# Optimization experiments

Measured on AMD Instinct MI355X. Metric: run time of the kernel, lower is better.

Reference implementation:

```python
import jax, jax.numpy as jnp
import numpy as np

B, S, E, H = 1, 2048, 1024, 16
D = E // H          # head_dim = 64
SM_SCALE = 0.5      # module default, not 1/sqrt(D)


def setup_inputs() -> dict:
    key = jax.random.key(0)
    ks = jax.random.split(key, 9)
    std = 0.02
    return {
        "x":  jax.random.normal(ks[0], (B, S, E), dtype=jnp.float32),
        "Wq": jax.random.normal(ks[1], (E, E), dtype=jnp.float32) * std,
        "bq": jnp.zeros((E,), dtype=jnp.float32),
        "Wk": jax.random.normal(ks[2], (E, E), dtype=jnp.float32) * std,
        "bk": jnp.zeros((E,), dtype=jnp.float32),
        "Wv": jax.random.normal(ks[3], (E, E), dtype=jnp.float32) * std,
        "bv": jnp.zeros((E,), dtype=jnp.float32),
        "Wo": jax.random.normal(ks[4], (E, E), dtype=jnp.float32) * std,
        "bo": jnp.zeros((E,), dtype=jnp.float32),
    }


def _split_heads(t):
    # [B,S,E] -> [B,H,S,D]
    b, s, _ = t.shape
    return jnp.transpose(t.reshape(b, s, H, D), (0, 2, 1, 3))


def reference(x, Wq, bq, Wk, bk, Wv, bv, Wo, bo):
    # Projections in fp32, then cast to bf16 (matches module's .astype(bf16))
    q = _split_heads((x @ Wq + bq).astype(jnp.bfloat16))
    k = _split_heads((x @ Wk + bk).astype(jnp.bfloat16))
    v = _split_heads((x @ Wv + bv).astype(jnp.bfloat16))

    # Blockwise loop in the original is mathematically full causal attention
    scores = jnp.einsum("bhqd,bhkd->bhqk", q, k) * SM_SCALE  # [B,H,S,S] bf16
    causal = jnp.tril(jnp.ones((S, S), dtype=bool))
    scores = jnp.where(causal[None, None, :, :], scores, -jnp.inf)
    probs = jax.nn.softmax(scores, axis=-1)
    out = jnp.einsum("bhqk,bhkd->bhqd", probs, v)            # [B,H,S,D]

    out = jnp.transpose(out, (0, 2, 1, 3)).reshape(B, S, E)
    # dropout off (is_training=False / rate=0); final projection in fp32
    return out.astype(jnp.float32) @ Wo + bo
```

## Files before the change

### kernel.cpp

```cpp
#include <hip/hip_runtime.h>
#include <hip/hip_bf16.h>

#define S_LEN 2048
#define E_DIM 1024
#define NH    16
#define HD    64
#define SM_SCALE 0.5f

typedef short bf16x8_t  __attribute__((ext_vector_type(8)));
typedef float f32x4_t   __attribute__((ext_vector_type(4)));
typedef float f32x16_t  __attribute__((ext_vector_type(16)));
typedef __bf16 bf16x4_t __attribute__((ext_vector_type(4)));

static __device__ __forceinline__ unsigned short f2bf_bits(float f) {
    return __builtin_bit_cast(unsigned short, (__bf16)f);
}

static __device__ __forceinline__ unsigned int cvt_pk_bf16(float lo, float hi) {
    unsigned int r;
    asm("v_cvt_pk_bf16_f32 %0, %1, %2" : "=v"(r) : "v"(lo), "v"(hi));
    return r;
}

#define GLD16(gp, lp) __builtin_amdgcn_global_load_lds(                       \
    (const __attribute__((address_space(1))) void*)(gp),                      \
    (__attribute__((address_space(3))) void*)(lp), 16, 0, 0)

__global__ void k_prep(const float* __restrict__ x,
                       const float* __restrict__ Wq, const float* __restrict__ Wk,
                       const float* __restrict__ Wv, const float* __restrict__ Wo,
                       __bf16* __restrict__ xb, __bf16* __restrict__ wt) {
    const int z = blockIdx.z;
    if (z < 4) {
        __shared__ float tile[32][33];
        const float* W = z == 0 ? Wq : z == 1 ? Wk : z == 2 ? Wv : Wo;
        __bf16* o = wt + (size_t)z * E_DIM * E_DIM;
        const int tx = threadIdx.x, ty = threadIdx.y;
        const int bx = blockIdx.x * 32, by = blockIdx.y * 32;
#pragma unroll
        for (int j = 0; j < 32; j += 8)
            tile[ty + j][tx] = W[(size_t)(by + ty + j) * E_DIM + bx + tx];
        __syncthreads();
#pragma unroll
        for (int j = 0; j < 32; j += 8)
            o[(size_t)(bx + ty + j) * E_DIM + by + tx] = (__bf16)tile[tx][ty + j];
    } else {
        const int bid = (z - 4) * 1024 + blockIdx.y * 32 + blockIdx.x;
        const int tid = threadIdx.y * 32 + threadIdx.x;
        const int i = bid * 256 + tid;
        const float4 v = ((const float4*)x)[i];
        bf16x4_t o4;
        o4.x = (__bf16)v.x; o4.y = (__bf16)v.y; o4.z = (__bf16)v.z; o4.w = (__bf16)v.w;
        ((bf16x4_t*)xb)[i] = o4;
    }
}

__global__ __launch_bounds__(256) void k_gemm_qkv(
    const __bf16* __restrict__ xb, const __bf16* __restrict__ wt,
    const float* __restrict__ bq, const float* __restrict__ bk, const float* __restrict__ bv,
    __bf16* __restrict__ qkv) {
    __shared__ __align__(16) unsigned short As[128 * 32];
    __shared__ __align__(16) unsigned short Bs[128 * 32];

    const int z = blockIdx.z;
    const __bf16* Bt = wt + (size_t)z * E_DIM * E_DIM;
    const float* bias = z == 0 ? bq : z == 1 ? bk : bv;
    __bf16* out = qkv + (size_t)z * NH * S_LEN * HD;

    const int tid = threadIdx.x, w = tid >> 6, l = tid & 63;
    const int lm = l & 15, q4 = l >> 4;
    const int bm = blockIdx.y, bn = blockIdx.x;
    const int wm = w >> 1, wn = w & 1;

    const int sm = (w << 4) + (l >> 2);
    const int skk = (l & 3) << 3;
    const __bf16* Ag = xb + (size_t)(bm * 128 + sm) * E_DIM + skk;
    const __bf16* Bg = Bt + (size_t)(bn * 128 + sm) * E_DIM + skk;
    unsigned short* AsW = As + (w << 9);
    unsigned short* BsW = Bs + (w << 9);

    f32x4_t acc[4][4];
#pragma unroll
    for (int i = 0; i < 4; i++)
#pragma unroll
        for (int j = 0; j < 4; j++) { acc[i][j].x = 0.f; acc[i][j].y = 0.f; acc[i][j].z = 0.f; acc[i][j].w = 0.f; }

    for (int k0 = 0; k0 < E_DIM; k0 += 32) {
        __syncthreads();
        GLD16(Ag + k0, AsW);
        GLD16(Ag + (size_t)64 * E_DIM + k0, AsW + 2048);
        GLD16(Bg + k0, BsW);
        GLD16(Bg + (size_t)64 * E_DIM + k0, BsW + 2048);
        __syncthreads();

        bf16x8_t af[4], bfr[4];
#pragma unroll
        for (int mt = 0; mt < 4; mt++)
            af[mt] = *(const bf16x8_t*)&As[(wm * 64 + mt * 16 + lm) * 32 + q4 * 8];
#pragma unroll
        for (int nt = 0; nt < 4; nt++)
            bfr[nt] = *(const bf16x8_t*)&Bs[(wn * 64 + nt * 16 + lm) * 32 + q4 * 8];
#pragma unroll
        for (int mt = 0; mt < 4; mt++)
#pragma unroll
            for (int nt = 0; nt < 4; nt++)
                acc[mt][nt] = __builtin_amdgcn_mfma_f32_16x16x32_bf16(af[mt], bfr[nt], acc[mt][nt], 0, 0, 0);
    }

#pragma unroll
    for (int nt = 0; nt < 4; nt++) {
        const int n = bn * 128 + wn * 64 + nt * 16 + lm;
        const float bval = bias[n];
        const int h = n >> 6, d = n & 63;
        const int tile0 = bm * 2 + wm;
        if (z == 2) {
            const int db = d >> 5, dl = d & 31;
#pragma unroll
            for (int mt = 0; mt < 4; mt++) {
                __bf16* ob = out + (((size_t)h * 32 + tile0) * 8 + db * 4 + mt) * 512
                                 + (dl + (q4 >> 1) * 32) * 8 + (q4 & 1) * 4;
                union { unsigned short s4[4]; uint2 u; } pk;
#pragma unroll
                for (int i = 0; i < 4; i++) pk.s4[i] = f2bf_bits(acc[mt][nt][i] + bval);
                *(uint2*)ob = pk.u;
            }
        } else {
            const float scale = (z == 0) ? SM_SCALE : 1.0f;
            const int kc = d >> 4, khalf = (d >> 3) & 1, j = d & 7;
#pragma unroll
            for (int mt = 0; mt < 4; mt++) {
                __bf16* ob = out + (((size_t)h * 32 + tile0) * 8 + (mt >> 1) * 4 + kc) * 512
                                 + ((mt & 1) * 16 + q4 * 4 + khalf * 32) * 8 + j;
#pragma unroll
                for (int i = 0; i < 4; i++)
                    ob[i * 8] = (__bf16)((acc[mt][nt][i] + bval) * scale);
            }
        }
    }
}

__global__ __launch_bounds__(256, 2) void k_attn(
    const __bf16* __restrict__ Qf, const __bf16* __restrict__ Kf, const __bf16* __restrict__ Vf,
    __bf16* __restrict__ attn) {
    __shared__ __align__(16) unsigned short KVs[2][2][4096];

    const int b = blockIdx.x;
    int qt, h;
    if (b < 256) { qt = 16 + (b >> 4); h = b & 15; }
    else         { qt = 15 - ((b - 256) >> 4); h = (b - 256) & 15; }

    const int tid = threadIdx.x, w = tid >> 6, l = tid & 63;
    const int rh = w & 1, kh = w >> 1;
    const int l31 = l & 31, lh = l >> 5;

    const __bf16* Qb = Qf + ((size_t)h * 32 + qt) * 4096;
    const __bf16* Kb = Kf + (size_t)h * 32 * 4096;
    const __bf16* Vb = Vf + (size_t)h * 32 * 4096;

    bf16x8_t qf[4];
#pragma unroll
    for (int kc = 0; kc < 4; kc++)
        qf[kc] = *(const bf16x8_t*)(Qb + ((rh * 4 + kc) << 9) + l * 8);

    float lacc = 0.f;
    f32x16_t oacc[2];
#pragma unroll
    for (int db = 0; db < 2; db++)
#pragma unroll
        for (int r = 0; r < 16; r++) oacc[db][r] = 0.f;

    GLD16(Kb + (w << 9) + l * 8,       &KVs[0][0][(w << 9) + l * 8]);
    GLD16(Kb + ((w + 4) << 9) + l * 8, &KVs[0][0][((w + 4) << 9) + l * 8]);
    GLD16(Vb + (w << 9) + l * 8,       &KVs[0][1][(w << 9) + l * 8]);
    GLD16(Vb + ((w + 4) << 9) + l * 8, &KVs[0][1][((w + 4) << 9) + l * 8]);
    __syncthreads();

    for (int s = 0; s <= qt; s++) {
        const int bb = s & 1;
        if (s < qt) {
            const __bf16* Kg = Kb + (size_t)(s + 1) * 4096;
            const __bf16* Vg = Vb + (size_t)(s + 1) * 4096;
            GLD16(Kg + (w << 9) + l * 8,       &KVs[bb ^ 1][0][(w << 9) + l * 8]);
            GLD16(Kg + ((w + 4) << 9) + l * 8, &KVs[bb ^ 1][0][((w + 4) << 9) + l * 8]);
            GLD16(Vg + (w << 9) + l * 8,       &KVs[bb ^ 1][1][(w << 9) + l * 8]);
            GLD16(Vg + ((w + 4) << 9) + l * 8, &KVs[bb ^ 1][1][((w + 4) << 9) + l * 8]);
        }

        const bool diag = (s == qt);
        if (!(diag && kh > rh)) {
            f32x16_t st;
#pragma unroll
            for (int r = 0; r < 16; r++) st[r] = 0.f;
            __builtin_amdgcn_s_setprio(1);
#pragma unroll
            for (int kc = 0; kc < 4; kc++) {
                bf16x8_t kf = *(const bf16x8_t*)&KVs[bb][0][((kh * 4 + kc) << 9) + l * 8];
                st = __builtin_amdgcn_mfma_f32_32x32x16_bf16(kf, qf[kc], st, 0, 0, 0);
            }
            __builtin_amdgcn_s_setprio(0);
            if (diag && kh == rh) {
#pragma unroll
                for (int r = 0; r < 16; r++) {
                    const int keyl = (r & 3) + 8 * (r >> 2) + 4 * lh;
                    st[r] = (keyl > l31) ? 0.f : __expf(st[r]);
                }
            } else {
#pragma unroll
                for (int r = 0; r < 16; r++) st[r] = __expf(st[r]);
            }
#pragma unroll
            for (int r = 0; r < 16; r++) lacc += st[r];
#pragma unroll
            for (int c = 0; c < 2; c++) {
                unsigned int v0 = cvt_pk_bf16(st[c * 8 + 0], st[c * 8 + 1]);
                unsigned int v1 = cvt_pk_bf16(st[c * 8 + 2], st[c * 8 + 3]);
                unsigned int v2 = cvt_pk_bf16(st[c * 8 + 4], st[c * 8 + 5]);
                unsigned int v3 = cvt_pk_bf16(st[c * 8 + 6], st[c * 8 + 7]);
                asm("v_permlane32_swap_b32 %0, %1" : "+v"(v0), "+v"(v2));
                asm("v_permlane32_swap_b32 %0, %1" : "+v"(v1), "+v"(v3));
                union { unsigned int u4[4]; bf16x8_t v; } pku;
                pku.u4[0] = v0; pku.u4[1] = v1; pku.u4[2] = v2; pku.u4[3] = v3;
                __builtin_amdgcn_s_setprio(1);
#pragma unroll
                for (int db = 0; db < 2; db++) {
                    bf16x8_t vf = *(const bf16x8_t*)&KVs[bb][1][((db * 4 + kh * 2 + c) << 9) + l * 8];
                    oacc[db] = __builtin_amdgcn_mfma_f32_32x32x16_bf16(vf, pku.v, oacc[db], 0, 0, 0);
                }
                __builtin_amdgcn_s_setprio(0);
            }
        }
        __syncthreads();
    }

    __syncthreads();
    float* Ex = (float*)KVs;
    if (kh == 1) {
        float* e = Ex + (rh * 64 + l) * 34;
#pragma unroll
        for (int db = 0; db < 2; db++)
#pragma unroll
            for (int r = 0; r < 16; r++) e[db * 16 + r] = oacc[db][r];
        e[32] = lacc;
    }
    __syncthreads();
    if (kh == 0) {
        const float* e = Ex + (rh * 64 + l) * 34;
#pragma unroll
        for (int db = 0; db < 2; db++)
#pragma unroll
            for (int r = 0; r < 16; r++) oacc[db][r] += e[db * 16 + r];
        lacc += e[32];
        lacc += __shfl_xor(lacc, 32, 64);
        const float rl = 1.f / lacc;
        const int row = qt * 64 + rh * 32 + l31;
#pragma unroll
        for (int db = 0; db < 2; db++)
#pragma unroll
            for (int a = 0; a < 4; a++) {
                union { unsigned short s4[4]; uint2 u; } pk;
#pragma unroll
                for (int i = 0; i < 4; i++) pk.s4[i] = f2bf_bits(oacc[db][a * 4 + i] * rl);
                *(uint2*)(attn + (size_t)row * E_DIM + h * HD + db * 32 + a * 8 + lh * 4) = pk.u;
            }
    }
}

__global__ __launch_bounds__(256) void k_gemm_out(
    const __bf16* __restrict__ A, const __bf16* __restrict__ Bt,
    const float* __restrict__ bias, float* __restrict__ out) {
    __shared__ __align__(16) unsigned short As[2][64 * 32];
    __shared__ __align__(16) unsigned short Bs[2][128 * 32];

    const int tid = threadIdx.x, w = tid >> 6, l = tid & 63;
    const int lm = l & 15, q4 = l >> 4;
    const int bm = blockIdx.y, bn = blockIdx.x;
    const int wm = w >> 1, wn = w & 1;

    const int sm = (w << 4) + (l >> 2);
    const int skk = (l & 3) << 3;
    const __bf16* Ag = A + (size_t)(bm * 64 + sm) * E_DIM + skk;
    const __bf16* Bg = Bt + (size_t)(bn * 128 + sm) * E_DIM + skk;
    const int woff = w << 9;

    f32x4_t acc[2][4];
#pragma unroll
    for (int i = 0; i < 2; i++)
#pragma unroll
        for (int j = 0; j < 4; j++) { acc[i][j].x = 0.f; acc[i][j].y = 0.f; acc[i][j].z = 0.f; acc[i][j].w = 0.f; }

    GLD16(Ag, &As[0][woff]);
    GLD16(Bg, &Bs[0][woff]);
    GLD16(Bg + (size_t)64 * E_DIM, &Bs[0][woff + 2048]);
    __syncthreads();

    for (int s = 0; s < 32; s++) {
        const int bb = s & 1;
        if (s < 31) {
            const int k0 = (s + 1) * 32;
            GLD16(Ag + k0, &As[bb ^ 1][woff]);
            GLD16(Bg + k0, &Bs[bb ^ 1][woff]);
            GLD16(Bg + (size_t)64 * E_DIM + k0, &Bs[bb ^ 1][woff + 2048]);
        }

        bf16x8_t af[2], bfr[4];
#pragma unroll
        for (int mt = 0; mt < 2; mt++)
            af[mt] = *(const bf16x8_t*)&As[bb][(wm * 32 + mt * 16 + lm) * 32 + q4 * 8];
#pragma unroll
        for (int nt = 0; nt < 4; nt++)
            bfr[nt] = *(const bf16x8_t*)&Bs[bb][(wn * 64 + nt * 16 + lm) * 32 + q4 * 8];
#pragma unroll
        for (int mt = 0; mt < 2; mt++)
#pragma unroll
            for (int nt = 0; nt < 4; nt++)
                acc[mt][nt] = __builtin_amdgcn_mfma_f32_16x16x32_bf16(af[mt], bfr[nt], acc[mt][nt], 0, 0, 0);
        __syncthreads();
    }

#pragma unroll
    for (int nt = 0; nt < 4; nt++) {
        const int n = bn * 128 + wn * 64 + nt * 16 + lm;
        const float bval = bias[n];
#pragma unroll
        for (int mt = 0; mt < 2; mt++) {
            const int r0 = bm * 64 + wm * 32 + mt * 16 + q4 * 4;
#pragma unroll
            for (int i = 0; i < 4; i++)
                out[(size_t)(r0 + i) * E_DIM + n] = acc[mt][nt][i] + bval;
        }
    }
}

extern "C" void kernel_launch(void* const* d_in, const int* in_sizes, int n_in,
                              void* d_out, int out_size, void* d_ws, size_t ws_size,
                              hipStream_t stream) {
    const float* x  = (const float*)d_in[0];
    const float* Wq = (const float*)d_in[1];
    const float* bq = (const float*)d_in[2];
    const float* Wk = (const float*)d_in[3];
    const float* bk = (const float*)d_in[4];
    const float* Wv = (const float*)d_in[5];
    const float* bv = (const float*)d_in[6];
    const float* Wo = (const float*)d_in[7];
    const float* bo = (const float*)d_in[8];
    float* out = (float*)d_out;

    char* ws = (char*)d_ws;
    __bf16* xb   = (__bf16*)(ws);
    __bf16* wt   = (__bf16*)(ws + ((size_t)4  << 20));
    __bf16* qkv  = (__bf16*)(ws + ((size_t)12 << 20));
    __bf16* attn = (__bf16*)(ws + ((size_t)24 << 20));

    k_prep<<<dim3(32, 32, 6), dim3(32, 8), 0, stream>>>(x, Wq, Wk, Wv, Wo, xb, wt);
    k_gemm_qkv<<<dim3(E_DIM / 128, S_LEN / 128, 3), 256, 0, stream>>>(xb, wt, bq, bk, bv, qkv);
    k_attn<<<dim3(512), 256, 0, stream>>>(
        qkv, qkv + (size_t)NH * S_LEN * HD, qkv + (size_t)2 * NH * S_LEN * HD, attn);
    k_gemm_out<<<dim3(E_DIM / 128, S_LEN / 64), 256, 0, stream>>>(
        attn, wt + (size_t)3 * E_DIM * E_DIM, bo, out);
}
```

Baseline: 145.6 us.

## Triple-buffer LDS loads with vmcnt waits and single barrier per iteration

The QKV GEMM, attention and output GEMM kernels move from single or double buffering to a three-stage LDS ring filled by global_load_lds two tiles ahead. Each iteration waits with an explicit s_waitcnt vmcnt for only the oldest tile, then issues one s_barrier instead of two __syncthreads. The aim is to hide global load latency and halve barrier count. It raises LDS use, which can lower occupancy in k_attn (launch bounds 256,2). The hand-written vmcnt counts and the removed trailing barrier risk races if the compiler emits other memory ops in between.

```diff
diff --git a/kernel.cpp b/kernel.cpp
--- a/kernel.cpp
+++ b/kernel.cpp
@@ -25,6 +25,8 @@
 #define GLD16(gp, lp) __builtin_amdgcn_global_load_lds(                       \
     (const __attribute__((address_space(1))) void*)(gp),                      \
     (__attribute__((address_space(3))) void*)(lp), 16, 0, 0)
+
+#define WAITVM(N) asm volatile("s_waitcnt vmcnt(" #N ")" ::: "memory")
 
 __global__ void k_prep(const float* __restrict__ x,
                        const float* __restrict__ Wq, const float* __restrict__ Wk,
@@ -59,8 +61,8 @@
     const __bf16* __restrict__ xb, const __bf16* __restrict__ wt,
     const float* __restrict__ bq, const float* __restrict__ bk, const float* __restrict__ bv,
     __bf16* __restrict__ qkv) {
-    __shared__ __align__(16) unsigned short As[128 * 32];
-    __shared__ __align__(16) unsigned short Bs[128 * 32];
+    __shared__ __align__(16) unsigned short As[3][4096];
+    __shared__ __align__(16) unsigned short Bs[3][4096];
 
     const int z = blockIdx.z;
     const __bf16* Bt = wt + (size_t)z * E_DIM * E_DIM;
@@ -76,8 +78,16 @@
     const int skk = (l & 3) << 3;
     const __bf16* Ag = xb + (size_t)(bm * 128 + sm) * E_DIM + skk;
     const __bf16* Bg = Bt + (size_t)(bn * 128 + sm) * E_DIM + skk;
-    unsigned short* AsW = As + (w << 9);
-    unsigned short* BsW = Bs + (w << 9);
+    const int woff = w << 9;
+
+    auto stage = [&](int t) {
+        const int buf = t % 3;
+        const int kk = t * 32;
+        GLD16(Ag + kk,                        &As[buf][woff]);
+        GLD16(Ag + (size_t)64 * E_DIM + kk,   &As[buf][woff + 2048]);
+        GLD16(Bg + kk,                        &Bs[buf][woff]);
+        GLD16(Bg + (size_t)64 * E_DIM + kk,   &Bs[buf][woff + 2048]);
+    };
 
     f32x4_t acc[4][4];
 #pragma unroll
@@ -85,21 +95,23 @@
 #pragma unroll
         for (int j = 0; j < 4; j++) { acc[i][j].x = 0.f; acc[i][j].y = 0.f; acc[i][j].z = 0.f; acc[i][j].w = 0.f; }
 
-    for (int k0 = 0; k0 < E_DIM; k0 += 32) {
-        __syncthreads();
-        GLD16(Ag + k0, AsW);
-        GLD16(Ag + (size_t)64 * E_DIM + k0, AsW + 2048);
-        GLD16(Bg + k0, BsW);
-        GLD16(Bg + (size_t)64 * E_DIM + k0, BsW + 2048);
-        __syncthreads();
+    stage(0);
+    stage(1);
+
+    for (int k = 0; k < 32; k++) {
+        const int bb = k % 3;
+        if (k < 31) WAITVM(4);
+        else        WAITVM(0);
+        __builtin_amdgcn_s_barrier();
+        if (k + 2 < 32) stage(k + 2);
 
         bf16x8_t af[4], bfr[4];
 #pragma unroll
         for (int mt = 0; mt < 4; mt++)
-            af[mt] = *(const bf16x8_t*)&As[(wm * 64 + mt * 16 + lm) * 32 + q4 * 8];
+            af[mt] = *(const bf16x8_t*)&As[bb][(wm * 64 + mt * 16 + lm) * 32 + q4 * 8];
 #pragma unroll
         for (int nt = 0; nt < 4; nt++)
-            bfr[nt] = *(const bf16x8_t*)&Bs[(wn * 64 + nt * 16 + lm) * 32 + q4 * 8];
+            bfr[nt] = *(const bf16x8_t*)&Bs[bb][(wn * 64 + nt * 16 + lm) * 32 + q4 * 8];
 #pragma unroll
         for (int mt = 0; mt < 4; mt++)
 #pragma unroll
@@ -142,7 +154,7 @@
 __global__ __launch_bounds__(256, 2) void k_attn(
     const __bf16* __restrict__ Qf, const __bf16* __restrict__ Kf, const __bf16* __restrict__ Vf,
     __bf16* __restrict__ attn) {
-    __shared__ __align__(16) unsigned short KVs[2][2][4096];
+    __shared__ __align__(16) unsigned short KVs[3][2][4096];
 
     const int b = blockIdx.x;
     int qt, h;
@@ -157,6 +169,16 @@
     const __bf16* Kb = Kf + (size_t)h * 32 * 4096;
     const __bf16* Vb = Vf + (size_t)h * 32 * 4096;
 
+    auto stage = [&](int t) {
+        const int buf = t % 3;
+        const __bf16* Kg = Kb + (size_t)t * 4096;
+        const __bf16* Vg = Vb + (size_t)t * 4096;
+        GLD16(Kg + (w << 9) + l * 8,       &KVs[buf][0][(w << 9) + l * 8]);
+        GLD16(Kg + ((w + 4) << 9) + l * 8, &KVs[buf][0][((w + 4) << 9) + l * 8]);
+        GLD16(Vg + (w << 9) + l * 8,       &KVs[buf][1][(w << 9) + l * 8]);
+        GLD16(Vg + ((w + 4) << 9) + l * 8, &KVs[buf][1][((w + 4) << 9) + l * 8]);
+    };
+
     bf16x8_t qf[4];
 #pragma unroll
     for (int kc = 0; kc < 4; kc++)
@@ -169,22 +191,16 @@
 #pragma unroll
         for (int r = 0; r < 16; r++) oacc[db][r] = 0.f;
 
-    GLD16(Kb + (w << 9) + l * 8,       &KVs[0][0][(w << 9) + l * 8]);
-    GLD16(Kb + ((w + 4) << 9) + l * 8, &KVs[0][0][((w + 4) << 9) + l * 8]);
-    GLD16(Vb + (w << 9) + l * 8,       &KVs[0][1][(w << 9) + l * 8]);
-    GLD16(Vb + ((w + 4) << 9) + l * 8, &KVs[0][1][((w + 4) << 9) + l * 8]);
-    __syncthreads();
+    WAITVM(0);
+    stage(0);
+    if (qt >= 1) stage(1);
 
     for (int s = 0; s <= qt; s++) {
-        const int bb = s & 1;
-        if (s < qt) {
-            const __bf16* Kg = Kb + (size_t)(s + 1) * 4096;
-            const __bf16* Vg = Vb + (size_t)(s + 1) * 4096;
-            GLD16(Kg + (w << 9) + l * 8,       &KVs[bb ^ 1][0][(w << 9) + l * 8]);
-            GLD16(Kg + ((w + 4) << 9) + l * 8, &KVs[bb ^ 1][0][((w + 4) << 9) + l * 8]);
-            GLD16(Vg + (w << 9) + l * 8,       &KVs[bb ^ 1][1][(w << 9) + l * 8]);
-            GLD16(Vg + ((w + 4) << 9) + l * 8, &KVs[bb ^ 1][1][((w + 4) << 9) + l * 8]);
-        }
+        const int bb = s % 3;
+        if (s < qt) WAITVM(4);
+        else        WAITVM(0);
+        __builtin_amdgcn_s_barrier();
+        if (s + 2 <= qt) stage(s + 2);
 
         const bool diag = (s == qt);
         if (!(diag && kh > rh)) {
@@ -229,7 +245,6 @@
                 __builtin_amdgcn_s_setprio(0);
             }
         }
-        __syncthreads();
     }
 
     __syncthreads();
@@ -268,8 +283,8 @@
 __global__ __launch_bounds__(256) void k_gemm_out(
     const __bf16* __restrict__ A, const __bf16* __restrict__ Bt,
     const float* __restrict__ bias, float* __restrict__ out) {
-    __shared__ __align__(16) unsigned short As[2][64 * 32];
-    __shared__ __align__(16) unsigned short Bs[2][128 * 32];
+    __shared__ __align__(16) unsigned short As[3][2048];
+    __shared__ __align__(16) unsigned short Bs[3][4096];
 
     const int tid = threadIdx.x, w = tid >> 6, l = tid & 63;
     const int lm = l & 15, q4 = l >> 4;
@@ -282,25 +297,29 @@
     const __bf16* Bg = Bt + (size_t)(bn * 128 + sm) * E_DIM + skk;
     const int woff = w << 9;
 
+    auto stage = [&](int t) {
+        const int buf = t % 3;
+        const int kk = t * 32;
+        GLD16(Ag + kk,                      &As[buf][woff]);
+        GLD16(Bg + kk,                      &Bs[buf][woff]);
+        GLD16(Bg + (size_t)64 * E_DIM + kk, &Bs[buf][woff + 2048]);
+    };
+
     f32x4_t acc[2][4];
 #pragma unroll
     for (int i = 0; i < 2; i++)
 #pragma unroll
         for (int j = 0; j < 4; j++) { acc[i][j].x = 0.f; acc[i][j].y = 0.f; acc[i][j].z = 0.f; acc[i][j].w = 0.f; }
 
-    GLD16(Ag, &As[0][woff]);
-    GLD16(Bg, &Bs[0][woff]);
-    GLD16(Bg + (size_t)64 * E_DIM, &Bs[0][woff + 2048]);
-    __syncthreads();
+    stage(0);
+    stage(1);
 
     for (int s = 0; s < 32; s++) {
-        const int bb = s & 1;
-        if (s < 31) {
-            const int k0 = (s + 1) * 32;
-            GLD16(Ag + k0, &As[bb ^ 1][woff]);
-            GLD16(Bg + k0, &Bs[bb ^ 1][woff]);
-            GLD16(Bg + (size_t)64 * E_DIM + k0, &Bs[bb ^ 1][woff + 2048]);
-        }
+        const int bb = s % 3;
+        if (s < 31) WAITVM(3);
+        else        WAITVM(0);
+        __builtin_amdgcn_s_barrier();
+        if (s + 2 < 32) stage(s + 2);
 
         bf16x8_t af[2], bfr[4];
 #pragma unroll
@@ -314,7 +333,6 @@
 #pragma unroll
             for (int nt = 0; nt < 4; nt++)
                 acc[mt][nt] = __builtin_amdgcn_mfma_f32_16x16x32_bf16(af[mt], bfr[nt], acc[mt][nt], 0, 0, 0);
-        __syncthreads();
     }
 
 #pragma unroll
```

New measurement: 159.5 us. 9.5% more time.

## Triple-buffer K/V tiles and software-pipeline QK^T one tile ahead of PV

Applied to the files above, without the earlier changes.

Moves the K/V shared-memory staging from a double buffer to a triple buffer, prefetching two tiles ahead. The loop is also software-pipelined so the QK^T MFMAs for tile s+1 are issued before the exp/PV work for tile s, using ping-pong score registers. This is meant to overlap the matrix work with the transcendental and pack work and to hide global-to-LDS latency. In exchange it uses more LDS (48KB per block) and more registers, which may hurt the two-blocks-per-CU occupancy.

```diff
diff --git a/kernel.cpp b/kernel.cpp
--- a/kernel.cpp
+++ b/kernel.cpp
@@ -142,7 +142,7 @@
 __global__ __launch_bounds__(256, 2) void k_attn(
     const __bf16* __restrict__ Qf, const __bf16* __restrict__ Kf, const __bf16* __restrict__ Vf,
     __bf16* __restrict__ attn) {
-    __shared__ __align__(16) unsigned short KVs[2][2][4096];
+    __shared__ __align__(16) unsigned short KVs[3][2][4096];
 
     const int b = blockIdx.x;
     int qt, h;
@@ -157,6 +157,16 @@
     const __bf16* Kb = Kf + (size_t)h * 32 * 4096;
     const __bf16* Vb = Vf + (size_t)h * 32 * 4096;
 
+    auto stage = [&](int t) {
+        const int buf = t % 3;
+        const __bf16* Kg = Kb + (size_t)t * 4096;
+        const __bf16* Vg = Vb + (size_t)t * 4096;
+        GLD16(Kg + (w << 9) + l * 8,       &KVs[buf][0][(w << 9) + l * 8]);
+        GLD16(Kg + ((w + 4) << 9) + l * 8, &KVs[buf][0][((w + 4) << 9) + l * 8]);
+        GLD16(Vg + (w << 9) + l * 8,       &KVs[buf][1][(w << 9) + l * 8]);
+        GLD16(Vg + ((w + 4) << 9) + l * 8, &KVs[buf][1][((w + 4) << 9) + l * 8]);
+    };
+
     bf16x8_t qf[4];
 #pragma unroll
     for (int kc = 0; kc < 4; kc++)
@@ -169,70 +179,76 @@
 #pragma unroll
         for (int r = 0; r < 16; r++) oacc[db][r] = 0.f;
 
-    GLD16(Kb + (w << 9) + l * 8,       &KVs[0][0][(w << 9) + l * 8]);
-    GLD16(Kb + ((w + 4) << 9) + l * 8, &KVs[0][0][((w + 4) << 9) + l * 8]);
-    GLD16(Vb + (w << 9) + l * 8,       &KVs[0][1][(w << 9) + l * 8]);
-    GLD16(Vb + ((w + 4) << 9) + l * 8, &KVs[0][1][((w + 4) << 9) + l * 8]);
+    auto qkt = [&](f32x16_t& dst, int t) {
+        const int bbq = t % 3;
+#pragma unroll
+        for (int r = 0; r < 16; r++) dst[r] = 0.f;
+        __builtin_amdgcn_s_setprio(1);
+#pragma unroll
+        for (int kc = 0; kc < 4; kc++) {
+            bf16x8_t kf = *(const bf16x8_t*)&KVs[bbq][0][((kh * 4 + kc) << 9) + l * 8];
+            dst = __builtin_amdgcn_mfma_f32_32x32x16_bf16(kf, qf[kc], dst, 0, 0, 0);
+        }
+        __builtin_amdgcn_s_setprio(0);
+    };
+
+    auto finish = [&](f32x16_t& st, int s) {
+        const bool diag = (s == qt);
+        if (diag && kh > rh) return;
+        if (diag && kh == rh) {
+#pragma unroll
+            for (int r = 0; r < 16; r++) {
+                const int keyl = (r & 3) + 8 * (r >> 2) + 4 * lh;
+                st[r] = (keyl > l31) ? 0.f : __expf(st[r]);
+            }
+        } else {
+#pragma unroll
+            for (int r = 0; r < 16; r++) st[r] = __expf(st[r]);
+        }
+#pragma unroll
+        for (int r = 0; r < 16; r++) lacc += st[r];
+        const int bbv = s % 3;
+#pragma unroll
+        for (int c = 0; c < 2; c++) {
+            unsigned int v0 = cvt_pk_bf16(st[c * 8 + 0], st[c * 8 + 1]);
+            unsigned int v1 = cvt_pk_bf16(st[c * 8 + 2], st[c * 8 + 3]);
+            unsigned int v2 = cvt_pk_bf16(st[c * 8 + 4], st[c * 8 + 5]);
+            unsigned int v3 = cvt_pk_bf16(st[c * 8 + 6], st[c * 8 + 7]);
+            asm("v_permlane32_swap_b32 %0, %1" : "+v"(v0), "+v"(v2));
+            asm("v_permlane32_swap_b32 %0, %1" : "+v"(v1), "+v"(v3));
+            union { unsigned int u4[4]; bf16x8_t v; } pku;
+            pku.u4[0] = v0; pku.u4[1] = v1; pku.u4[2] = v2; pku.u4[3] = v3;
+            __builtin_amdgcn_s_setprio(1);
+#pragma unroll
+            for (int db = 0; db < 2; db++) {
+                bf16x8_t vf = *(const bf16x8_t*)&KVs[bbv][1][((db * 4 + kh * 2 + c) << 9) + l * 8];
+                oacc[db] = __builtin_amdgcn_mfma_f32_32x32x16_bf16(vf, pku.v, oacc[db], 0, 0, 0);
+            }
+            __builtin_amdgcn_s_setprio(0);
+        }
+    };
+
+    stage(0);
     __syncthreads();
-
-    for (int s = 0; s <= qt; s++) {
-        const int bb = s & 1;
-        if (s < qt) {
-            const __bf16* Kg = Kb + (size_t)(s + 1) * 4096;
-            const __bf16* Vg = Vb + (size_t)(s + 1) * 4096;
-            GLD16(Kg + (w << 9) + l * 8,       &KVs[bb ^ 1][0][(w << 9) + l * 8]);
-            GLD16(Kg + ((w + 4) << 9) + l * 8, &KVs[bb ^ 1][0][((w + 4) << 9) + l * 8]);
-            GLD16(Vg + (w << 9) + l * 8,       &KVs[bb ^ 1][1][(w << 9) + l * 8]);
-            GLD16(Vg + ((w + 4) << 9) + l * 8, &KVs[bb ^ 1][1][((w + 4) << 9) + l * 8]);
-        }
-
-        const bool diag = (s == qt);
-        if (!(diag && kh > rh)) {
-            f32x16_t st;
-#pragma unroll
-            for (int r = 0; r < 16; r++) st[r] = 0.f;
-            __builtin_amdgcn_s_setprio(1);
-#pragma unroll
-            for (int kc = 0; kc < 4; kc++) {
-                bf16x8_t kf = *(const bf16x8_t*)&KVs[bb][0][((kh * 4 + kc) << 9) + l * 8];
-                st = __builtin_amdgcn_mfma_f32_32x32x16_bf16(kf, qf[kc], st, 0, 0, 0);
-            }
-            __builtin_amdgcn_s_setprio(0);
-            if (diag && kh == rh) {
-#pragma unroll
-                for (int r = 0; r < 16; r++) {
-                    const int keyl = (r & 3) + 8 * (r >> 2) + 4 * lh;
-                    st[r] = (keyl > l31) ? 0.f : __expf(st[r]);
-                }
-            } else {
-#pragma unroll
-                for (int r = 0; r < 16; r++) st[r] = __expf(st[r]);
-            }
-#pragma unroll
-            for (int r = 0; r < 16; r++) lacc += st[r];
-#pragma unroll
-            for (int c = 0; c < 2; c++) {
-                unsigned int v0 = cvt_pk_bf16(st[c * 8 + 0], st[c * 8 + 1]);
-                unsigned int v1 = cvt_pk_bf16(st[c * 8 + 2], st[c * 8 + 3]);
-                unsigned int v2 = cvt_pk_bf16(st[c * 8 + 4], st[c * 8 + 5]);
-                unsigned int v3 = cvt_pk_bf16(st[c * 8 + 6], st[c * 8 + 7]);
-                asm("v_permlane32_swap_b32 %0, %1" : "+v"(v0), "+v"(v2));
-                asm("v_permlane32_swap_b32 %0, %1" : "+v"(v1), "+v"(v3));
-                union { unsigned int u4[4]; bf16x8_t v; } pku;
-                pku.u4[0] = v0; pku.u4[1] = v1; pku.u4[2] = v2; pku.u4[3] = v3;
-                __builtin_amdgcn_s_setprio(1);
-#pragma unroll
-                for (int db = 0; db < 2; db++) {
-                    bf16x8_t vf = *(const bf16x8_t*)&KVs[bb][1][((db * 4 + kh * 2 + c) << 9) + l * 8];
-                    oacc[db] = __builtin_amdgcn_mfma_f32_32x32x16_bf16(vf, pku.v, oacc[db], 0, 0, 0);
-                }
-                __builtin_amdgcn_s_setprio(0);
-            }
-        }
-        __syncthreads();
-    }
-
+    if (qt >= 1) stage(1);
+    f32x16_t stA, stB;
+    qkt(stA, 0);
     __syncthreads();
+
+    int s = 0;
+    while (true) {
+        if (s + 2 <= qt) stage(s + 2);
+        if (s < qt) qkt(stB, s + 1);
+        finish(stA, s);
+        __syncthreads();
+        if (++s > qt) break;
+        if (s + 2 <= qt) stage(s + 2);
+        if (s < qt) qkt(stA, s + 1);
+        finish(stB, s);
+        __syncthreads();
+        if (++s > qt) break;
+    }
+
     float* Ex = (float*)KVs;
     if (kh == 1) {
         float* e = Ex + (rh * 64 + l) * 34;
```

Result: slower. 152.0 us (+4.4%).

## Double KV tile to 128 keys per iteration with two interleaved score MFMAs

Applied to the files above, without the earlier changes.

The attention loop now stages 128 keys of K and V per iteration instead of 64, so there are half as many barrier-separated steps. Each wave issues two independent QK MFMA chains, giving the hardware more instruction-level parallelism. The causal mask is generalised to cover partial diagonal tiles. In exchange, shared memory per block doubles, which may limit occupancy, and the final tile can do more wasted or masked work.

```diff
diff --git a/kernel.cpp b/kernel.cpp
--- a/kernel.cpp
+++ b/kernel.cpp
@@ -142,7 +142,7 @@
 __global__ __launch_bounds__(256, 2) void k_attn(
     const __bf16* __restrict__ Qf, const __bf16* __restrict__ Kf, const __bf16* __restrict__ Vf,
     __bf16* __restrict__ attn) {
-    __shared__ __align__(16) unsigned short KVs[2][2][4096];
+    __shared__ __align__(16) unsigned short KVs[2][2][8192];
 
     const int b = blockIdx.x;
     int qt, h;
@@ -157,6 +157,17 @@
     const __bf16* Kb = Kf + (size_t)h * 32 * 4096;
     const __bf16* Vb = Vf + (size_t)h * 32 * 4096;
 
+    auto stage = [&](int t, int buf) {
+        const __bf16* Kg = Kb + (size_t)t * 8192;
+        const __bf16* Vg = Vb + (size_t)t * 8192;
+#pragma unroll
+        for (int i = 0; i < 4; i++) {
+            const int ch = (w + i * 4) << 9;
+            GLD16(Kg + ch + l * 8, &KVs[buf][0][ch + l * 8]);
+            GLD16(Vg + ch + l * 8, &KVs[buf][1][ch + l * 8]);
+        }
+    };
+
     bf16x8_t qf[4];
 #pragma unroll
     for (int kc = 0; kc < 4; kc++)
@@ -169,66 +180,72 @@
 #pragma unroll
         for (int r = 0; r < 16; r++) oacc[db][r] = 0.f;
 
-    GLD16(Kb + (w << 9) + l * 8,       &KVs[0][0][(w << 9) + l * 8]);
-    GLD16(Kb + ((w + 4) << 9) + l * 8, &KVs[0][0][((w + 4) << 9) + l * 8]);
-    GLD16(Vb + (w << 9) + l * 8,       &KVs[0][1][(w << 9) + l * 8]);
-    GLD16(Vb + ((w + 4) << 9) + l * 8, &KVs[0][1][((w + 4) << 9) + l * 8]);
+    stage(0, 0);
     __syncthreads();
 
-    for (int s = 0; s <= qt; s++) {
-        const int bb = s & 1;
-        if (s < qt) {
-            const __bf16* Kg = Kb + (size_t)(s + 1) * 4096;
-            const __bf16* Vg = Vb + (size_t)(s + 1) * 4096;
-            GLD16(Kg + (w << 9) + l * 8,       &KVs[bb ^ 1][0][(w << 9) + l * 8]);
-            GLD16(Kg + ((w + 4) << 9) + l * 8, &KVs[bb ^ 1][0][((w + 4) << 9) + l * 8]);
-            GLD16(Vg + (w << 9) + l * 8,       &KVs[bb ^ 1][1][(w << 9) + l * 8]);
-            GLD16(Vg + ((w + 4) << 9) + l * 8, &KVs[bb ^ 1][1][((w + 4) << 9) + l * 8]);
-        }
-
-        const bool diag = (s == qt);
-        if (!(diag && kh > rh)) {
-            f32x16_t st;
-#pragma unroll
-            for (int r = 0; r < 16; r++) st[r] = 0.f;
+    const int ntiles = (qt >> 1) + 1;
+    const int rowmin = qt * 64 + rh * 32;
+
+    auto finish = [&](f32x16_t& st, int bb, int sub, int base, bool tri) {
+        if (tri) {
+            const int off = rowmin - base;
+#pragma unroll
+            for (int r = 0; r < 16; r++) {
+                const int keyl = (r & 3) + 8 * (r >> 2) + 4 * lh;
+                st[r] = (keyl > l31 + off) ? 0.f : __expf(st[r]);
+            }
+        } else {
+#pragma unroll
+            for (int r = 0; r < 16; r++) st[r] = __expf(st[r]);
+        }
+#pragma unroll
+        for (int r = 0; r < 16; r++) lacc += st[r];
+#pragma unroll
+        for (int c = 0; c < 2; c++) {
+            unsigned int v0 = cvt_pk_bf16(st[c * 8 + 0], st[c * 8 + 1]);
+            unsigned int v1 = cvt_pk_bf16(st[c * 8 + 2], st[c * 8 + 3]);
+            unsigned int v2 = cvt_pk_bf16(st[c * 8 + 4], st[c * 8 + 5]);
+            unsigned int v3 = cvt_pk_bf16(st[c * 8 + 6], st[c * 8 + 7]);
+            asm("v_permlane32_swap_b32 %0, %1" : "+v"(v0), "+v"(v2));
+            asm("v_permlane32_swap_b32 %0, %1" : "+v"(v1), "+v"(v3));
+            union { unsigned int u4[4]; bf16x8_t v; } pku;
+            pku.u4[0] = v0; pku.u4[1] = v1; pku.u4[2] = v2; pku.u4[3] = v3;
             __builtin_amdgcn_s_setprio(1);
 #pragma unroll
-            for (int kc = 0; kc < 4; kc++) {
-                bf16x8_t kf = *(const bf16x8_t*)&KVs[bb][0][((kh * 4 + kc) << 9) + l * 8];
-                st = __builtin_amdgcn_mfma_f32_32x32x16_bf16(kf, qf[kc], st, 0, 0, 0);
+            for (int db = 0; db < 2; db++) {
+                bf16x8_t vf = *(const bf16x8_t*)
+                    &KVs[bb][1][((kh * 8 + db * 4 + sub * 2 + c) << 9) + l * 8];
+                oacc[db] = __builtin_amdgcn_mfma_f32_32x32x16_bf16(vf, pku.v, oacc[db], 0, 0, 0);
             }
             __builtin_amdgcn_s_setprio(0);
-            if (diag && kh == rh) {
-#pragma unroll
-                for (int r = 0; r < 16; r++) {
-                    const int keyl = (r & 3) + 8 * (r >> 2) + 4 * lh;
-                    st[r] = (keyl > l31) ? 0.f : __expf(st[r]);
-                }
-            } else {
-#pragma unroll
-                for (int r = 0; r < 16; r++) st[r] = __expf(st[r]);
-            }
-#pragma unroll
-            for (int r = 0; r < 16; r++) lacc += st[r];
-#pragma unroll
-            for (int c = 0; c < 2; c++) {
-                unsigned int v0 = cvt_pk_bf16(st[c * 8 + 0], st[c * 8 + 1]);
-                unsigned int v1 = cvt_pk_bf16(st[c * 8 + 2], st[c * 8 + 3]);
-                unsigned int v2 = cvt_pk_bf16(st[c * 8 + 4], st[c * 8 + 5]);
-                unsigned int v3 = cvt_pk_bf16(st[c * 8 + 6], st[c * 8 + 7]);
-                asm("v_permlane32_swap_b32 %0, %1" : "+v"(v0), "+v"(v2));
-                asm("v_permlane32_swap_b32 %0, %1" : "+v"(v1), "+v"(v3));
-                union { unsigned int u4[4]; bf16x8_t v; } pku;
-                pku.u4[0] = v0; pku.u4[1] = v1; pku.u4[2] = v2; pku.u4[3] = v3;
-                __builtin_amdgcn_s_setprio(1);
-#pragma unroll
-                for (int db = 0; db < 2; db++) {
-                    bf16x8_t vf = *(const bf16x8_t*)&KVs[bb][1][((db * 4 + kh * 2 + c) << 9) + l * 8];
-                    oacc[db] = __builtin_amdgcn_mfma_f32_32x32x16_bf16(vf, pku.v, oacc[db], 0, 0, 0);
-                }
-                __builtin_amdgcn_s_setprio(0);
-            }
-        }
+        }
+    };
+
+    for (int t = 0; t < ntiles; t++) {
+        const int bb = t & 1;
+        if (t + 1 < ntiles) stage(t + 1, bb ^ 1);
+
+        const bool last = (t == ntiles - 1);
+        const int base0 = t * 128 + kh * 64;
+        const bool d0 = !last || (base0      <= rowmin + 31);
+        const bool d1 = !last || (base0 + 32 <= rowmin + 31);
+
+        f32x16_t st0, st1;
+#pragma unroll
+        for (int r = 0; r < 16; r++) { st0[r] = 0.f; st1[r] = 0.f; }
+        __builtin_amdgcn_s_setprio(1);
+#pragma unroll
+        for (int kc = 0; kc < 4; kc++) {
+            bf16x8_t kf0 = *(const bf16x8_t*)&KVs[bb][0][((kh * 8 +     kc) << 9) + l * 8];
+            bf16x8_t kf1 = *(const bf16x8_t*)&KVs[bb][0][((kh * 8 + 4 + kc) << 9) + l * 8];
+            st0 = __builtin_amdgcn_mfma_f32_32x32x16_bf16(kf0, qf[kc], st0, 0, 0, 0);
+            st1 = __builtin_amdgcn_mfma_f32_32x32x16_bf16(kf1, qf[kc], st1, 0, 0, 0);
+        }
+        __builtin_amdgcn_s_setprio(0);
+
+        if (d0) finish(st0, bb, 0, base0,      last && (base0 + 31 > rowmin));
+        if (d1) finish(st1, bb, 1, base0 + 32, last && (base0 + 63 > rowmin));
+
         __syncthreads();
     }
 
```

Result: no change. 146.0 us (+0.3%).
